# Performance work log

Measured on AMD Instinct MI355X. Metric: run time of the kernel, lower is better.

The kernel has to match this reference:

```python
import jax, jax.numpy as jnp
import numpy as np

N_NODES = 100000


def _gcn_norm(edge_index, edge_weight, n):
    # PyG GCNConv default: add self-loops (weight 1), symmetric normalization
    src, dst = edge_index[0], edge_index[1]
    loop = jnp.arange(n, dtype=src.dtype)
    src = jnp.concatenate([src, loop])
    dst = jnp.concatenate([dst, loop])
    w = jnp.concatenate([edge_weight, jnp.ones((n,), edge_weight.dtype)])
    deg = jax.ops.segment_sum(w, dst, num_segments=n)  # in-degree incl. self-loop
    dinv = jnp.where(deg > 0, jax.lax.rsqrt(deg), 0.0)
    norm = dinv[src] * w * dinv[dst]  # D^-1/2 A D^-1/2 edge values
    return src, dst, norm


def _gcn_conv(h, src, dst, norm, W, b, n):
    # linear transform then edge gather -> scale -> scatter-add
    h = h @ W                                   # [n, out]
    out = jax.ops.segment_sum(norm[:, None] * h[src], dst, num_segments=n)
    return out + b


def setup_inputs() -> dict:
    key = jax.random.key(0)
    ks = jax.random.split(key, 6)
    n, f, h3, c, e = N_NODES, 512, 16, 8, 3200000
    x = jax.random.normal(ks[0], (n, f), dtype=jnp.float32)
    edge_index = jax.random.randint(ks[1], (2, e), 0, n, dtype=jnp.int64)
    edge_weight = jax.random.uniform(ks[2], (e,), dtype=jnp.float32)
    W1 = jax.random.normal(ks[3], (f, h3), dtype=jnp.float32) / np.sqrt(f)
    b1 = jnp.zeros((h3,), jnp.float32)
    W2 = jax.random.normal(ks[4], (h3, c), dtype=jnp.float32) / np.sqrt(h3)
    b2 = jnp.zeros((c,), jnp.float32)
    return {"x": x, "edge_index": edge_index, "edge_weight": edge_weight,
            "W1": W1, "b1": b1, "W2": W2, "b2": b2}


def reference(x, edge_index, edge_weight, W1, b1, W2, b2):
    n = x.shape[0]
    # cached=True: same normalized adjacency is reused by both layers
    src, dst, norm = _gcn_norm(edge_index, edge_weight, n)
    h = jax.nn.relu(_gcn_conv(x, src, dst, norm, W1, b1, n))
    # dropout is identity in eval mode
    h = _gcn_conv(h, src, dst, norm, W2, b2, n)
    return jax.nn.log_softmax(h, axis=1)
```

## Files before the change

### kernel.cpp

```cpp
#include <hip/hip_runtime.h>
#include <hip/hip_bf16.h>
#include <hip/hip_fp16.h>
#include <math.h>


#define NBLK 1024
#define MAX_NBK 2048
#define CAP_SORTED 3072

typedef _Float16 half8 __attribute__((ext_vector_type(8)));
typedef __fp16 fp16x2 __attribute__((ext_vector_type(2)));
typedef float f32x4 __attribute__((ext_vector_type(4)));

#define XPITCH 136

__device__ __forceinline__ float2 h2f(unsigned u) {
    __half2 h = *reinterpret_cast<__half2*>(&u);
    return __half22float2(h);
}

__global__ __launch_bounds__(256) void k_hist(const int* __restrict__ dst,
                                              int* __restrict__ bh,
                                              int NBK, int E, int chunk) {
    __shared__ int hist[MAX_NBK];
    int blk = blockIdx.x, tid = threadIdx.x;
    for (int b = tid; b < NBK; b += 256) hist[b] = 0;
    __syncthreads();
    int lo = blk * chunk, hi = min(lo + chunk, E);
    for (int e = lo + tid; e < hi; e += 256) atomicAdd(&hist[dst[e] >> 6], 1);
    __syncthreads();
    for (int b = tid; b < NBK; b += 256) bh[(size_t)blk * NBK + b] = hist[b];
}

__global__ __launch_bounds__(256) void k_colscan(int* __restrict__ bh,
                                                 int* __restrict__ totals, int NBK) {
    __shared__ int s[256];
    int b = blockIdx.x, t = threadIdx.x;
    int v0 = bh[(size_t)(4 * t + 0) * NBK + b];
    int v1 = bh[(size_t)(4 * t + 1) * NBK + b];
    int v2 = bh[(size_t)(4 * t + 2) * NBK + b];
    int v3 = bh[(size_t)(4 * t + 3) * NBK + b];
    int lsum = v0 + v1 + v2 + v3;
    s[t] = lsum;
    __syncthreads();
    for (int off = 1; off < 256; off <<= 1) {
        int u = (t >= off) ? s[t - off] : 0;
        __syncthreads();
        s[t] += u;
        __syncthreads();
    }
    int pre = s[t] - lsum;
    bh[(size_t)(4 * t + 0) * NBK + b] = pre;
    bh[(size_t)(4 * t + 1) * NBK + b] = pre + v0;
    bh[(size_t)(4 * t + 2) * NBK + b] = pre + v0 + v1;
    bh[(size_t)(4 * t + 3) * NBK + b] = pre + v0 + v1 + v2;
    if (t == 255) totals[b] = s[255];
}

__global__ __launch_bounds__(256) void k_scan_totals(const int* __restrict__ totals,
                                                     int* __restrict__ bs,
                                                     int NBK, int E) {
    __shared__ int s[256];
    int t = threadIdx.x;
    int chunk = (NBK + 255) >> 8;
    int lo = t * chunk, hi = min(lo + chunk, NBK);
    int acc = 0;
    for (int i = lo; i < hi; ++i) acc += totals[i];
    s[t] = acc;
    __syncthreads();
    for (int off = 1; off < 256; off <<= 1) {
        int u = (t >= off) ? s[t - off] : 0;
        __syncthreads();
        s[t] += u;
        __syncthreads();
    }
    int pre = (t == 0) ? 0 : s[t - 1];
    for (int i = lo; i < hi; ++i) { bs[i] = pre; pre += totals[i]; }
    if (t == 0) bs[NBK] = E;
}

__global__ __launch_bounds__(256) void k_bin(const int* __restrict__ src,
                                             const int* __restrict__ dst,
                                             const float* __restrict__ w,
                                             const int* __restrict__ bh,
                                             const int* __restrict__ bs,
                                             uint2* __restrict__ ebuf,
                                             int NBK, int E, int chunk) {
    __shared__ int cur[MAX_NBK];
    int blk = blockIdx.x, tid = threadIdx.x;
    for (int b = tid; b < NBK; b += 256)
        cur[b] = bs[b] + bh[(size_t)blk * NBK + b];
    __syncthreads();
    int lo = blk * chunk, hi = min(lo + chunk, E);
    for (int e = lo + tid; e < hi; e += 256) {
        int d = dst[e];
        int b = d >> 6;
        int pos = atomicAdd(&cur[b], 1);
        ebuf[pos] = make_uint2((unsigned)src[e] | ((unsigned)(d & 63) << 20),
                               __float_as_uint(w[e]));
    }
}

__global__ __launch_bounds__(256) void k_sortdeg(uint2* __restrict__ ebuf,
                                                 const int* __restrict__ bs,
                                                 int* __restrict__ nrp,
                                                 float* __restrict__ dinv,
                                                 int n, int NBK, int E) {
    __shared__ uint2 stage[CAP_SORTED];
    __shared__ int cnt[64];
    __shared__ float dw[64];
    __shared__ int cur[64];
    int b = blockIdx.x, tid = threadIdx.x;
    if (tid < 64) { cnt[tid] = 0; dw[tid] = 1.0f; }
    __syncthreads();
    int e0 = bs[b], e1 = bs[b + 1];
    int m = e1 - e0;
    bool sorted = (m <= CAP_SORTED);
    if (sorted) {
        for (int i = tid; i < m; i += 256) {
            uint2 p = ebuf[e0 + i];
            stage[i] = p;
            int dl = p.x >> 20;
            atomicAdd(&cnt[dl], 1);
            atomicAdd(&dw[dl], __uint_as_float(p.y));
        }
    } else {
        for (int i = tid; i < m; i += 256) {
            uint2 p = ebuf[e0 + i];
            int dl = p.x >> 20;
            atomicAdd(&cnt[dl], 1);
            atomicAdd(&dw[dl], __uint_as_float(p.y));
        }
    }
    __syncthreads();
    if (tid < 64) {
        int v = cnt[tid], x = v;
#pragma unroll
        for (int off = 1; off < 64; off <<= 1) {
            int y = __shfl_up(x, off);
            if (tid >= off) x += y;
        }
        int pre = x - v;
        cur[tid] = pre;
        int node = b * 64 + tid;
        if (node < n) {
            nrp[node] = e0 + pre;
            dinv[node] = rsqrtf(dw[tid]);
        }
    }
    if (b == NBK - 1 && tid == 0) nrp[n] = E;
    __syncthreads();
    if (sorted) {
        for (int i = tid; i < m; i += 256) {
            uint2 p = stage[i];
            int dl = p.x >> 20;
            int pos = atomicAdd(&cur[dl], 1);
            ebuf[e0 + pos] = p;
        }
    }
}

__global__ __launch_bounds__(256) void k_prepW(const float* __restrict__ W1,
                                               _Float16* __restrict__ W1h) {
    int idx = blockIdx.x * 256 + threadIdx.x;
    if (idx < 512 * 16) {
        int k = idx >> 4, c = idx & 15;
        W1h[c * 512 + k] = (_Float16)W1[idx];
    }
}

__global__ __launch_bounds__(256) void k_gemm1(const float* __restrict__ x,
                                               const _Float16* __restrict__ W1h,
                                               const float* __restrict__ dinv,
                                               __half* __restrict__ g1, int n) {
    __shared__ _Float16 xlds[64 * XPITCH];
    int tid = threadIdx.x;
    int wave = tid >> 6, lane = tid & 63;
    int col = lane & 15;
    int kgrp = lane >> 4;
    const half8* wcol = (const half8*)(W1h + (size_t)col * 512);
    half8 bfrag[16];
#pragma unroll
    for (int t = 0; t < 16; ++t) bfrag[t] = wcol[t * 4 + kgrp];

    int rbase = blockIdx.x * 64;
    if (rbase >= n) return;
    int srow = tid >> 5;
    int sc4  = tid & 31;
    int rowl = wave * 16 + col;
    f32x4 acc = {0.f, 0.f, 0.f, 0.f};
#pragma unroll
    for (int c = 0; c < 4; ++c) {
#pragma unroll
        for (int i = 0; i < 8; ++i) {
            int row = srow + i * 8;
            int grow = min(rbase + row, n - 1);
            float4 v = *(const float4*)(x + (size_t)grow * 512 + c * 128 + sc4 * 4);
            union { fp16x2 h[2]; uint2 u; } pk;
            pk.h[0] = __builtin_amdgcn_cvt_pkrtz(v.x, v.y);
            pk.h[1] = __builtin_amdgcn_cvt_pkrtz(v.z, v.w);
            *(uint2*)(&xlds[row * XPITCH + sc4 * 4]) = pk.u;
        }
        __syncthreads();
#pragma unroll
        for (int s = 0; s < 4; ++s) {
            half8 a = *(const half8*)(&xlds[rowl * XPITCH + s * 32 + kgrp * 8]);
            acc = __builtin_amdgcn_mfma_f32_16x16x32_f16(a, bfrag[c * 4 + s], acc, 0, 0, 0);
        }
        __syncthreads();
    }
#pragma unroll
    for (int r = 0; r < 4; ++r) {
        int node = rbase + wave * 16 + kgrp * 4 + r;
        if (node < n) {
            float dv = dinv[node];
            g1[(size_t)node * 16 + col] = __float2half(acc[r] * dv);
        }
    }
}

__global__ __launch_bounds__(256) void k_agg16g2(const int* __restrict__ nrp,
                                                 const uint2* __restrict__ ebuf,
                                                 const int* __restrict__ bs,
                                                 const float* __restrict__ dinv,
                                                 const __half* __restrict__ g1,
                                                 const float* __restrict__ W2,
                                                 const float* __restrict__ b1,
                                                 __half* __restrict__ g2, int n) {
    __shared__ float acc[64 * 17];
    __shared__ float w2s[16 * 8];
    __shared__ float b1s[16];
    int b = blockIdx.x, tid = threadIdx.x;
    int nodeBase = b * 64;
    if (tid < 128) w2s[tid] = W2[tid];
    if (tid < 16) b1s[tid] = b1[tid];
    int e0b = bs[b], e1b = bs[b + 1];
    int m = e1b - e0b;
    if (m <= CAP_SORTED) {
        int l = tid >> 2, q = tid & 3;
        int node = nodeBase + l;
        float r[16];
#pragma unroll
        for (int k = 0; k < 16; ++k) r[k] = 0.f;
        int e = 0, eE = 0;
        if (node < n) {
            e = nrp[node] + q;
            eE = nrp[node + 1];
            if (q == 0) {
                const uint4* sr = (const uint4*)(g1 + (size_t)node * 16);
                uint4 s0 = sr[0], s1 = sr[1];
                float2 f;
                f = h2f(s0.x); r[0] = f.x;  r[1] = f.y;
                f = h2f(s0.y); r[2] = f.x;  r[3] = f.y;
                f = h2f(s0.z); r[4] = f.x;  r[5] = f.y;
                f = h2f(s0.w); r[6] = f.x;  r[7] = f.y;
                f = h2f(s1.x); r[8] = f.x;  r[9] = f.y;
                f = h2f(s1.y); r[10] = f.x; r[11] = f.y;
                f = h2f(s1.z); r[12] = f.x; r[13] = f.y;
                f = h2f(s1.w); r[14] = f.x; r[15] = f.y;
            }
        }
        for (; e < eE; e += 4) {
            uint2 p = ebuf[e];
            float wE = __uint_as_float(p.y);
            unsigned s = p.x & 0xFFFFF;
            const uint4* hr = (const uint4*)(g1 + (size_t)s * 16);
            uint4 a0 = hr[0], a1 = hr[1];
            float2 f;
            f = h2f(a0.x); r[0]  = fmaf(wE, f.x, r[0]);  r[1]  = fmaf(wE, f.y, r[1]);
            f = h2f(a0.y); r[2]  = fmaf(wE, f.x, r[2]);  r[3]  = fmaf(wE, f.y, r[3]);
            f = h2f(a0.z); r[4]  = fmaf(wE, f.x, r[4]);  r[5]  = fmaf(wE, f.y, r[5]);
            f = h2f(a0.w); r[6]  = fmaf(wE, f.x, r[6]);  r[7]  = fmaf(wE, f.y, r[7]);
            f = h2f(a1.x); r[8]  = fmaf(wE, f.x, r[8]);  r[9]  = fmaf(wE, f.y, r[9]);
            f = h2f(a1.y); r[10] = fmaf(wE, f.x, r[10]); r[11] = fmaf(wE, f.y, r[11]);
            f = h2f(a1.z); r[12] = fmaf(wE, f.x, r[12]); r[13] = fmaf(wE, f.y, r[13]);
            f = h2f(a1.w); r[14] = fmaf(wE, f.x, r[14]); r[15] = fmaf(wE, f.y, r[15]);
        }
        float s8[8];
#pragma unroll
        for (int k = 0; k < 8; ++k) {
            float tlo = __shfl_xor(r[k], 1);
            float thi = __shfl_xor(r[k + 8], 1);
            s8[k] = (q & 1) ? (r[k + 8] + thi) : (r[k] + tlo);
        }
        float s4[4];
#pragma unroll
        for (int k = 0; k < 4; ++k) {
            float tlo = __shfl_xor(s8[k], 2);
            float thi = __shfl_xor(s8[k + 4], 2);
            s4[k] = (q & 2) ? (s8[k + 4] + thi) : (s8[k] + tlo);
        }
        if (node < n) {
            int chbase = (q & 1) * 8 + ((q >> 1) & 1) * 4;
            float* ar = &acc[l * 17 + chbase];
            ar[0] = s4[0]; ar[1] = s4[1]; ar[2] = s4[2]; ar[3] = s4[3];
        }
    } else {
        for (int o = tid; o < 64 * 16; o += 256) {
            int l = o >> 4, c = o & 15;
            int node = nodeBase + l;
            float v = 0.f;
            if (node < n) v = __half2float(g1[(size_t)node * 16 + c]);
            acc[l * 17 + c] = v;
        }
        __syncthreads();
        for (int e = e0b + tid; e < e1b; e += 256) {
            uint2 p = ebuf[e];
            int s = p.x & 0xFFFFF;
            int dl = p.x >> 20;
            float wE = __uint_as_float(p.y);
            const uint4* hr = (const uint4*)(g1 + (size_t)s * 16);
            uint4 q0 = hr[0], q1 = hr[1];
            float* ar = &acc[dl * 17];
            float2 f;
            f = h2f(q0.x); atomicAdd(ar + 0,  wE * f.x); atomicAdd(ar + 1,  wE * f.y);
            f = h2f(q0.y); atomicAdd(ar + 2,  wE * f.x); atomicAdd(ar + 3,  wE * f.y);
            f = h2f(q0.z); atomicAdd(ar + 4,  wE * f.x); atomicAdd(ar + 5,  wE * f.y);
            f = h2f(q0.w); atomicAdd(ar + 6,  wE * f.x); atomicAdd(ar + 7,  wE * f.y);
            f = h2f(q1.x); atomicAdd(ar + 8,  wE * f.x); atomicAdd(ar + 9,  wE * f.y);
            f = h2f(q1.y); atomicAdd(ar + 10, wE * f.x); atomicAdd(ar + 11, wE * f.y);
            f = h2f(q1.z); atomicAdd(ar + 12, wE * f.x); atomicAdd(ar + 13, wE * f.y);
            f = h2f(q1.w); atomicAdd(ar + 14, wE * f.x); atomicAdd(ar + 15, wE * f.y);
        }
    }
    __syncthreads();
    for (int o = tid; o < 64 * 8; o += 256) {
        int l = o >> 3, cc = o & 7;
        int node = nodeBase + l;
        if (node >= n) continue;
        float dv = dinv[node];
        float s = 0.f;
#pragma unroll
        for (int k = 0; k < 16; ++k) {
            float v = fmaxf(fmaf(dv, acc[l * 17 + k], b1s[k]), 0.f);
            s = fmaf(v, w2s[k * 8 + cc], s);
        }
        g2[(size_t)node * 8 + cc] = __float2half(s * dv);
    }
}

__global__ __launch_bounds__(256) void k_agg8lsm(const int* __restrict__ nrp,
                                                 const uint2* __restrict__ ebuf,
                                                 const int* __restrict__ bs,
                                                 const float* __restrict__ dinv,
                                                 const __half* __restrict__ g2,
                                                 const float* __restrict__ b2,
                                                 float* __restrict__ out, int n) {
    __shared__ float acc[64 * 9];
    __shared__ float b2s[8];
    int b = blockIdx.x, tid = threadIdx.x;
    int nodeBase = b * 64;
    if (tid < 8) b2s[tid] = b2[tid];
    int e0b = bs[b], e1b = bs[b + 1];
    int m = e1b - e0b;
    if (m <= CAP_SORTED) {
        int l = tid >> 2, q = tid & 3;
        int node = nodeBase + l;
        float r[8];
#pragma unroll
        for (int k = 0; k < 8; ++k) r[k] = 0.f;
        int e = 0, eE = 0;
        if (node < n) {
            e = nrp[node] + q;
            eE = nrp[node + 1];
            if (q == 0) {
                const uint4* sr = (const uint4*)(g2 + (size_t)node * 8);
                uint4 s0 = sr[0];
                float2 f;
                f = h2f(s0.x); r[0] = f.x; r[1] = f.y;
                f = h2f(s0.y); r[2] = f.x; r[3] = f.y;
                f = h2f(s0.z); r[4] = f.x; r[5] = f.y;
                f = h2f(s0.w); r[6] = f.x; r[7] = f.y;
            }
        }
        for (; e < eE; e += 4) {
            uint2 p = ebuf[e];
            float wE = __uint_as_float(p.y);
            unsigned s = p.x & 0xFFFFF;
            const uint4* hr = (const uint4*)(g2 + (size_t)s * 8);
            uint4 a0 = hr[0];
            float2 f;
            f = h2f(a0.x); r[0] = fmaf(wE, f.x, r[0]); r[1] = fmaf(wE, f.y, r[1]);
            f = h2f(a0.y); r[2] = fmaf(wE, f.x, r[2]); r[3] = fmaf(wE, f.y, r[3]);
            f = h2f(a0.z); r[4] = fmaf(wE, f.x, r[4]); r[5] = fmaf(wE, f.y, r[5]);
            f = h2f(a0.w); r[6] = fmaf(wE, f.x, r[6]); r[7] = fmaf(wE, f.y, r[7]);
        }
        float s4[4];
#pragma unroll
        for (int k = 0; k < 4; ++k) {
            float tlo = __shfl_xor(r[k], 1);
            float thi = __shfl_xor(r[k + 4], 1);
            s4[k] = (q & 1) ? (r[k + 4] + thi) : (r[k] + tlo);
        }
        float s2[2];
#pragma unroll
        for (int k = 0; k < 2; ++k) {
            float tlo = __shfl_xor(s4[k], 2);
            float thi = __shfl_xor(s4[k + 2], 2);
            s2[k] = (q & 2) ? (s4[k + 2] + thi) : (s4[k] + tlo);
        }
        if (node < n) {
            int chbase = (q & 1) * 4 + ((q >> 1) & 1) * 2;
            acc[l * 9 + chbase] = s2[0];
            acc[l * 9 + chbase + 1] = s2[1];
        }
    } else {
        for (int o = tid; o < 64 * 8; o += 256) {
            int l = o >> 3, c = o & 7;
            int node = nodeBase + l;
            float v = 0.f;
            if (node < n) v = __half2float(g2[(size_t)node * 8 + c]);
            acc[l * 9 + c] = v;
        }
        __syncthreads();
        for (int e = e0b + tid; e < e1b; e += 256) {
            uint2 p = ebuf[e];
            int s = p.x & 0xFFFFF;
            int dl = p.x >> 20;
            float wE = __uint_as_float(p.y);
            const uint4* hr = (const uint4*)(g2 + (size_t)s * 8);
            uint4 q0 = hr[0];
            float* ar = &acc[dl * 9];
            float2 f;
            f = h2f(q0.x); atomicAdd(ar + 0, wE * f.x); atomicAdd(ar + 1, wE * f.y);
            f = h2f(q0.y); atomicAdd(ar + 2, wE * f.x); atomicAdd(ar + 3, wE * f.y);
            f = h2f(q0.z); atomicAdd(ar + 4, wE * f.x); atomicAdd(ar + 5, wE * f.y);
            f = h2f(q0.w); atomicAdd(ar + 6, wE * f.x); atomicAdd(ar + 7, wE * f.y);
        }
    }
    __syncthreads();
    if (tid < 64) {
        int node = nodeBase + tid;
        if (node < n) {
            float dv = dinv[node];
            float v[8];
#pragma unroll
            for (int cc = 0; cc < 8; ++cc) v[cc] = fmaf(dv, acc[tid * 9 + cc], b2s[cc]);
            float mx = v[0];
#pragma unroll
            for (int cc = 1; cc < 8; ++cc) mx = fmaxf(mx, v[cc]);
            float sum = 0.f;
#pragma unroll
            for (int cc = 0; cc < 8; ++cc) sum += expf(v[cc] - mx);
            float lg = mx + logf(sum);
#pragma unroll
            for (int cc = 0; cc < 8; ++cc) out[(size_t)node * 8 + cc] = v[cc] - lg;
        }
    }
}

__global__ void k_init_deg(float* __restrict__ deg, int n) {
    int i = blockIdx.x * blockDim.x + threadIdx.x;
    if (i < n) deg[i] = 1.0f;
}
__global__ void k_deg_scatter(const int* __restrict__ dst, const float* __restrict__ w,
                              float* __restrict__ deg, int E) {
    int e = blockIdx.x * blockDim.x + threadIdx.x;
    if (e < E) atomicAdd(&deg[dst[e]], w[e]);
}
__global__ void k_rsqrt_inplace(float* __restrict__ deg, int n) {
    int i = blockIdx.x * blockDim.x + threadIdx.x;
    if (i < n) { float d = deg[i]; deg[i] = d > 0.0f ? rsqrtf(d) : 0.0f; }
}
__global__ __launch_bounds__(256) void k_gemm1f(const float* __restrict__ x,
                                                const float* __restrict__ W1,
                                                float* __restrict__ h1, int n) {
    __shared__ float Wt[16 * 516];
    int tid = threadIdx.x;
    for (int idx = tid; idx < 512 * 16; idx += 256) {
        int k = idx >> 4, c = idx & 15;
        Wt[c * 516 + k] = W1[idx];
    }
    __syncthreads();
    int wave = tid >> 6, lane = tid & 63;
    int c = lane & 15, r = lane >> 4;
    int row = blockIdx.x * 16 + wave * 4 + r;
    if (row >= n) return;
    const float4* xr = (const float4*)(x + (size_t)row * 512);
    const float4* wr = (const float4*)(Wt + c * 516);
    float4 acc = make_float4(0.f, 0.f, 0.f, 0.f);
#pragma unroll 8
    for (int k4 = 0; k4 < 128; ++k4) {
        float4 xv = xr[k4];
        float4 wv = wr[k4];
        acc.x = fmaf(xv.x, wv.x, acc.x);
        acc.y = fmaf(xv.y, wv.y, acc.y);
        acc.z = fmaf(xv.z, wv.z, acc.z);
        acc.w = fmaf(xv.w, wv.w, acc.w);
    }
    h1[(size_t)row * 16 + c] = (acc.x + acc.y) + (acc.z + acc.w);
}
template <int CH>
__global__ void k_self_init(const float* __restrict__ dinv, const float* __restrict__ h,
                            float* __restrict__ agg, int n) {
    int t = blockIdx.x * blockDim.x + threadIdx.x;
    int i = t / CH;
    if (i < n) { float dv = dinv[i]; agg[t] = dv * dv * h[t]; }
}
template <int CH>
__global__ void k_scatter(const int* __restrict__ src, const int* __restrict__ dst,
                          const float* __restrict__ w, const float* __restrict__ dinv,
                          const float* __restrict__ h, float* __restrict__ agg, int E) {
    int t = blockIdx.x * blockDim.x + threadIdx.x;
    int e = t / CH, c = t % CH;
    if (e >= E) return;
    int s = src[e], d = dst[e];
    float nrm = dinv[s] * w[e] * dinv[d];
    atomicAdd(&agg[(size_t)d * CH + c], nrm * h[(size_t)s * CH + c]);
}
__global__ __launch_bounds__(256) void k_gemm2(const float* __restrict__ agg1,
                                               const float* __restrict__ b1,
                                               const float* __restrict__ W2,
                                               float* __restrict__ h2, int n) {
    __shared__ float w2s[16 * 8];
    __shared__ float b1s[16];
    int tid = threadIdx.x;
    if (tid < 128) w2s[tid] = W2[tid];
    if (tid < 16) b1s[tid] = b1[tid];
    __syncthreads();
    int t = blockIdx.x * 256 + tid;
    int i = t >> 3, cc = t & 7;
    if (i >= n) return;
    const float* a = agg1 + (size_t)i * 16;
    float acc = 0.f;
#pragma unroll
    for (int k = 0; k < 16; ++k) {
        float v = fmaxf(a[k] + b1s[k], 0.f);
        acc = fmaf(v, w2s[k * 8 + cc], acc);
    }
    h2[(size_t)i * 8 + cc] = acc;
}
__global__ void k_logsoftmax(float* __restrict__ out, const float* __restrict__ b2, int n) {
    int i = blockIdx.x * blockDim.x + threadIdx.x;
    if (i >= n) return;
    float v[8];
#pragma unroll
    for (int c = 0; c < 8; ++c) v[c] = out[(size_t)i * 8 + c] + b2[c];
    float m = v[0];
#pragma unroll
    for (int c = 1; c < 8; ++c) m = fmaxf(m, v[c]);
    float s = 0.f;
#pragma unroll
    for (int c = 0; c < 8; ++c) s += expf(v[c] - m);
    float l = m + logf(s);
#pragma unroll
    for (int c = 0; c < 8; ++c) out[(size_t)i * 8 + c] = v[c] - l;
}

static inline size_t align64(size_t v) { return (v + 63) & ~(size_t)63; }

extern "C" void kernel_launch(void* const* d_in, const int* in_sizes, int n_in,
                              void* d_out, int out_size, void* d_ws, size_t ws_size,
                              hipStream_t stream) {
    const float* x  = (const float*)d_in[0];
    const int*   ei = (const int*)d_in[1];
    const float* ew = (const float*)d_in[2];
    const float* W1 = (const float*)d_in[3];
    const float* b1 = (const float*)d_in[4];
    const float* W2 = (const float*)d_in[5];
    const float* b2 = (const float*)d_in[6];
    float* out      = (float*)d_out;

    const int n = in_sizes[0] / 512;
    const int E = in_sizes[2];
    const int* src = ei;
    const int* dst = ei + E;

    const int B = 256;
    const int NBK = (n + 63) >> 6;
    const int chunk = (E + NBLK - 1) / NBLK;

    size_t off_ebuf = 0;
    size_t off_h1   = align64(off_ebuf + (size_t)E * 8);
    size_t off_h2   = align64(off_h1 + (size_t)16 * n * 2);
    size_t off_bh   = align64(off_h2 + (size_t)8 * n * 2);
    size_t off_tot  = align64(off_bh + (size_t)NBLK * NBK * 4);
    size_t off_bs   = align64(off_tot + (size_t)NBK * 4);
    size_t off_dinv = align64(off_bs + (size_t)(NBK + 1) * 4);
    size_t off_nrp  = align64(off_dinv + (size_t)n * 4);
    size_t off_w1h  = align64(off_nrp + (size_t)(n + 1) * 4);
    size_t need     = off_w1h + (size_t)512 * 16 * 2;

    if (ws_size >= need && NBK <= MAX_NBK && n <= (1 << 20)) {
        char* ws = (char*)d_ws;
        uint2*    ebuf = (uint2*)(ws + off_ebuf);
        __half*   g1   = (__half*)(ws + off_h1);
        __half*   g2   = (__half*)(ws + off_h2);
        int*      bh   = (int*)(ws + off_bh);
        int*      tot  = (int*)(ws + off_tot);
        int*      bs   = (int*)(ws + off_bs);
        float*    dinv = (float*)(ws + off_dinv);
        int*      nrp  = (int*)(ws + off_nrp);
        _Float16* w1h  = (_Float16*)(ws + off_w1h);

        k_prepW<<<32, B, 0, stream>>>(W1, w1h);
        k_hist<<<NBLK, B, 0, stream>>>(dst, bh, NBK, E, chunk);
        k_colscan<<<NBK, B, 0, stream>>>(bh, tot, NBK);
        k_scan_totals<<<1, B, 0, stream>>>(tot, bs, NBK, E);
        k_bin<<<NBLK, B, 0, stream>>>(src, dst, ew, bh, bs, ebuf, NBK, E, chunk);
        k_sortdeg<<<NBK, B, 0, stream>>>(ebuf, bs, nrp, dinv, n, NBK, E);

        k_gemm1<<<(n + 63) / 64, B, 0, stream>>>(x, w1h, dinv, g1, n);
        k_agg16g2<<<NBK, B, 0, stream>>>(nrp, ebuf, bs, dinv, g1, W2, b1, g2, n);
        k_agg8lsm<<<NBK, B, 0, stream>>>(nrp, ebuf, bs, dinv, g2, b2, out, n);
    } else {
        float* deg  = (float*)d_ws;
        float* h1   = deg + n;
        float* h2   = h1;
        float* agg1 = h1 + (size_t)16 * n;
        int gn = (n + B - 1) / B, gE = (E + B - 1) / B;

        k_init_deg<<<gn, B, 0, stream>>>(deg, n);
        k_deg_scatter<<<gE, B, 0, stream>>>(dst, ew, deg, E);
        k_rsqrt_inplace<<<gn, B, 0, stream>>>(deg, n);
        k_gemm1f<<<(n + 15) / 16, B, 0, stream>>>(x, W1, h1, n);
        k_self_init<16><<<((size_t)16 * n + B - 1) / B, B, 0, stream>>>(deg, h1, agg1, n);
        k_scatter<16><<<((size_t)16 * E + B - 1) / B, B, 0, stream>>>(src, dst, ew, deg, h1, agg1, E);
        k_gemm2<<<((size_t)8 * n + B - 1) / B, B, 0, stream>>>(agg1, b1, W2, h2, n);
        k_self_init<8><<<((size_t)8 * n + B - 1) / B, B, 0, stream>>>(deg, h2, out, n);
        k_scatter<8><<<((size_t)8 * E + B - 1) / B, B, 0, stream>>>(src, dst, ew, deg, h2, out, E);
        k_logsoftmax<<<gn, B, 0, stream>>>(out, b2, n);
    }
}
```

Before: 248.3 us.

## Halve nodes per aggregation block and restructure column scan of bucket histograms

The two aggregation kernels now handle 32 nodes per block with 8 lanes per node instead of 64 nodes with 4 lanes. This doubles the block count and gives each node's edge list more parallel lanes, at the cost of one extra shuffle reduction stage. The overflow path filters edges to its half of the 64-node bucket, so each of the two blocks reads the whole bucket's edges. The column scan now has each thread serially sum 64 histogram rows across 16 buckets per block, which gives 16-wide coalesced reads and fewer blocks in place of the strided 256-thread tree scan.

```diff
diff --git a/kernel.cpp b/kernel.cpp
--- a/kernel.cpp
+++ b/kernel.cpp
@@ -35,26 +35,30 @@
 __global__ __launch_bounds__(256) void k_colscan(int* __restrict__ bh,
                                                  int* __restrict__ totals, int NBK) {
     __shared__ int s[256];
-    int b = blockIdx.x, t = threadIdx.x;
-    int v0 = bh[(size_t)(4 * t + 0) * NBK + b];
-    int v1 = bh[(size_t)(4 * t + 1) * NBK + b];
-    int v2 = bh[(size_t)(4 * t + 2) * NBK + b];
-    int v3 = bh[(size_t)(4 * t + 3) * NBK + b];
-    int lsum = v0 + v1 + v2 + v3;
-    s[t] = lsum;
-    __syncthreads();
-    for (int off = 1; off < 256; off <<= 1) {
-        int u = (t >= off) ? s[t - off] : 0;
-        __syncthreads();
-        s[t] += u;
-        __syncthreads();
-    }
-    int pre = s[t] - lsum;
-    bh[(size_t)(4 * t + 0) * NBK + b] = pre;
-    bh[(size_t)(4 * t + 1) * NBK + b] = pre + v0;
-    bh[(size_t)(4 * t + 2) * NBK + b] = pre + v0 + v1;
-    bh[(size_t)(4 * t + 3) * NBK + b] = pre + v0 + v1 + v2;
-    if (t == 255) totals[b] = s[255];
+    int tid = threadIdx.x;
+    int bk = tid & 15, r = tid >> 4;
+    int b = blockIdx.x * 16 + bk;
+    bool ok = (b < NBK);
+    int base = r * 64;
+    int lsum = 0;
+    if (ok) {
+        for (int j = 0; j < 64; ++j)
+            lsum += bh[(size_t)(base + j) * NBK + b];
+    }
+    s[r * 16 + bk] = lsum;
+    __syncthreads();
+    int pre = 0;
+    for (int i = 0; i < r; ++i) pre += s[i * 16 + bk];
+    if (ok) {
+        int run = pre;
+        for (int j = 0; j < 64; ++j) {
+            size_t idx = (size_t)(base + j) * NBK + b;
+            int v = bh[idx];
+            bh[idx] = run;
+            run += v;
+        }
+        if (r == 15) totals[b] = run;
+    }
 }
 
 __global__ __launch_bounds__(256) void k_scan_totals(const int* __restrict__ totals,
@@ -227,17 +231,18 @@
                                                  const float* __restrict__ W2,
                                                  const float* __restrict__ b1,
                                                  __half* __restrict__ g2, int n) {
-    __shared__ float acc[64 * 17];
+    __shared__ float acc[32 * 17];
     __shared__ float w2s[16 * 8];
     __shared__ float b1s[16];
-    int b = blockIdx.x, tid = threadIdx.x;
-    int nodeBase = b * 64;
+    int blk = blockIdx.x, tid = threadIdx.x;
+    int nodeBase = blk * 32;
     if (tid < 128) w2s[tid] = W2[tid];
     if (tid < 16) b1s[tid] = b1[tid];
-    int e0b = bs[b], e1b = bs[b + 1];
+    int bucket = blk >> 1;
+    int e0b = bs[bucket], e1b = bs[bucket + 1];
     int m = e1b - e0b;
     if (m <= CAP_SORTED) {
-        int l = tid >> 2, q = tid & 3;
+        int l = tid >> 3, q = tid & 7;
         int node = nodeBase + l;
         float r[16];
 #pragma unroll
@@ -260,7 +265,7 @@
                 f = h2f(s1.w); r[14] = f.x; r[15] = f.y;
             }
         }
-        for (; e < eE; e += 4) {
+        for (; e < eE; e += 8) {
             uint2 p = ebuf[e];
             float wE = __uint_as_float(p.y);
             unsigned s = p.x & 0xFFFFF;
@@ -290,13 +295,20 @@
             float thi = __shfl_xor(s8[k + 4], 2);
             s4[k] = (q & 2) ? (s8[k + 4] + thi) : (s8[k] + tlo);
         }
-        if (node < n) {
-            int chbase = (q & 1) * 8 + ((q >> 1) & 1) * 4;
-            float* ar = &acc[l * 17 + chbase];
-            ar[0] = s4[0]; ar[1] = s4[1]; ar[2] = s4[2]; ar[3] = s4[3];
+        float s2[2];
+#pragma unroll
+        for (int k = 0; k < 2; ++k) {
+            float tlo = __shfl_xor(s4[k], 4);
+            float thi = __shfl_xor(s4[k + 2], 4);
+            s2[k] = (q & 4) ? (s4[k + 2] + thi) : (s4[k] + tlo);
+        }
+        if (node < n) {
+            int chbase = (q & 1) * 8 + ((q >> 1) & 1) * 4 + ((q >> 2) & 1) * 2;
+            acc[l * 17 + chbase] = s2[0];
+            acc[l * 17 + chbase + 1] = s2[1];
         }
     } else {
-        for (int o = tid; o < 64 * 16; o += 256) {
+        for (int o = tid; o < 32 * 16; o += 256) {
             int l = o >> 4, c = o & 15;
             int node = nodeBase + l;
             float v = 0.f;
@@ -304,10 +316,12 @@
             acc[l * 17 + c] = v;
         }
         __syncthreads();
+        int half = (blk & 1) * 32;
         for (int e = e0b + tid; e < e1b; e += 256) {
             uint2 p = ebuf[e];
+            int dl = (int)(p.x >> 20) - half;
+            if (dl < 0 || dl >= 32) continue;
             int s = p.x & 0xFFFFF;
-            int dl = p.x >> 20;
             float wE = __uint_as_float(p.y);
             const uint4* hr = (const uint4*)(g1 + (size_t)s * 16);
             uint4 q0 = hr[0], q1 = hr[1];
@@ -324,18 +338,19 @@
         }
     }
     __syncthreads();
-    for (int o = tid; o < 64 * 8; o += 256) {
-        int l = o >> 3, cc = o & 7;
+    {
+        int l = tid >> 3, cc = tid & 7;
         int node = nodeBase + l;
-        if (node >= n) continue;
-        float dv = dinv[node];
-        float s = 0.f;
-#pragma unroll
-        for (int k = 0; k < 16; ++k) {
-            float v = fmaxf(fmaf(dv, acc[l * 17 + k], b1s[k]), 0.f);
-            s = fmaf(v, w2s[k * 8 + cc], s);
-        }
-        g2[(size_t)node * 8 + cc] = __float2half(s * dv);
+        if (node < n) {
+            float dv = dinv[node];
+            float s = 0.f;
+#pragma unroll
+            for (int k = 0; k < 16; ++k) {
+                float v = fmaxf(fmaf(dv, acc[l * 17 + k], b1s[k]), 0.f);
+                s = fmaf(v, w2s[k * 8 + cc], s);
+            }
+            g2[(size_t)node * 8 + cc] = __float2half(s * dv);
+        }
     }
 }
 
@@ -346,15 +361,16 @@
                                                  const __half* __restrict__ g2,
                                                  const float* __restrict__ b2,
                                                  float* __restrict__ out, int n) {
-    __shared__ float acc[64 * 9];
+    __shared__ float acc[32 * 9];
     __shared__ float b2s[8];
-    int b = blockIdx.x, tid = threadIdx.x;
-    int nodeBase = b * 64;
+    int blk = blockIdx.x, tid = threadIdx.x;
+    int nodeBase = blk * 32;
     if (tid < 8) b2s[tid] = b2[tid];
-    int e0b = bs[b], e1b = bs[b + 1];
+    int bucket = blk >> 1;
+    int e0b = bs[bucket], e1b = bs[bucket + 1];
     int m = e1b - e0b;
     if (m <= CAP_SORTED) {
-        int l = tid >> 2, q = tid & 3;
+        int l = tid >> 3, q = tid & 7;
         int node = nodeBase + l;
         float r[8];
 #pragma unroll
@@ -373,7 +389,7 @@
                 f = h2f(s0.w); r[6] = f.x; r[7] = f.y;
             }
         }
-        for (; e < eE; e += 4) {
+        for (; e < eE; e += 8) {
             uint2 p = ebuf[e];
             float wE = __uint_as_float(p.y);
             unsigned s = p.x & 0xFFFFF;
@@ -399,13 +415,18 @@
             float thi = __shfl_xor(s4[k + 2], 2);
             s2[k] = (q & 2) ? (s4[k + 2] + thi) : (s4[k] + tlo);
         }
-        if (node < n) {
-            int chbase = (q & 1) * 4 + ((q >> 1) & 1) * 2;
-            acc[l * 9 + chbase] = s2[0];
-            acc[l * 9 + chbase + 1] = s2[1];
+        float s1;
+        {
+            float tlo = __shfl_xor(s2[0], 4);
+            float thi = __shfl_xor(s2[1], 4);
+            s1 = (q & 4) ? (s2[1] + thi) : (s2[0] + tlo);
+        }
+        if (node < n) {
+            int ch = (q & 1) * 4 + ((q >> 1) & 1) * 2 + ((q >> 2) & 1);
+            acc[l * 9 + ch] = s1;
         }
     } else {
-        for (int o = tid; o < 64 * 8; o += 256) {
+        for (int o = tid; o < 32 * 8; o += 256) {
             int l = o >> 3, c = o & 7;
             int node = nodeBase + l;
             float v = 0.f;
@@ -413,10 +434,12 @@
             acc[l * 9 + c] = v;
         }
         __syncthreads();
+        int half = (blk & 1) * 32;
         for (int e = e0b + tid; e < e1b; e += 256) {
             uint2 p = ebuf[e];
+            int dl = (int)(p.x >> 20) - half;
+            if (dl < 0 || dl >= 32) continue;
             int s = p.x & 0xFFFFF;
-            int dl = p.x >> 20;
             float wE = __uint_as_float(p.y);
             const uint4* hr = (const uint4*)(g2 + (size_t)s * 8);
             uint4 q0 = hr[0];
@@ -429,7 +452,7 @@
         }
     }
     __syncthreads();
-    if (tid < 64) {
+    if (tid < 32) {
         int node = nodeBase + tid;
         if (node < n) {
             float dv = dinv[node];
@@ -568,6 +591,7 @@
 
     const int B = 256;
     const int NBK = (n + 63) >> 6;
+    const int NB32 = (n + 31) >> 5;
     const int chunk = (E + NBLK - 1) / NBLK;
 
     size_t off_ebuf = 0;
@@ -595,14 +619,14 @@
 
         k_prepW<<<32, B, 0, stream>>>(W1, w1h);
         k_hist<<<NBLK, B, 0, stream>>>(dst, bh, NBK, E, chunk);
-        k_colscan<<<NBK, B, 0, stream>>>(bh, tot, NBK);
+        k_colscan<<<(NBK + 15) / 16, B, 0, stream>>>(bh, tot, NBK);
         k_scan_totals<<<1, B, 0, stream>>>(tot, bs, NBK, E);
         k_bin<<<NBLK, B, 0, stream>>>(src, dst, ew, bh, bs, ebuf, NBK, E, chunk);
         k_sortdeg<<<NBK, B, 0, stream>>>(ebuf, bs, nrp, dinv, n, NBK, E);
 
         k_gemm1<<<(n + 63) / 64, B, 0, stream>>>(x, w1h, dinv, g1, n);
-        k_agg16g2<<<NBK, B, 0, stream>>>(nrp, ebuf, bs, dinv, g1, W2, b1, g2, n);
-        k_agg8lsm<<<NBK, B, 0, stream>>>(nrp, ebuf, bs, dinv, g2, b2, out, n);
+        k_agg16g2<<<NB32, B, 0, stream>>>(nrp, ebuf, bs, dinv, g1, W2, b1, g2, n);
+        k_agg8lsm<<<NB32, B, 0, stream>>>(nrp, ebuf, bs, dinv, g2, b2, out, n);
     } else {
         float* deg  = (float*)d_ws;
         float* h1   = deg + n;
```

New measurement: 228.8 us. -7.8%, faster.
